# Optimization experiments

Hardware: AMD Instinct MI355X
Metric: run time of the kernel (lower is better)

Reference implementation:

```python
import jax, jax.numpy as jnp
import numpy as np

B, S, H = 1, 2048, 2048
NH, NKV, HD = 32, 4, 128
G = NH // NKV            # query groups per kv head
EPS = 1e-6
THETA = 1000000.0


def _rmsnorm(x, w):
    # per-head RMSNorm over last (head_dim) axis
    var = jnp.mean(jnp.square(x), axis=-1, keepdims=True)
    return x * jax.lax.rsqrt(var + EPS) * w


def _rotate_half(x):
    x1, x2 = jnp.split(x, 2, axis=-1)
    return jnp.concatenate([-x2, x1], axis=-1)


def _rope(x, cos, sin):
    # x: [B,S,h,HD], cos/sin: [S,HD]
    c = cos[None, :, None, :]
    s = sin[None, :, None, :]
    return x * c + _rotate_half(x) * s


def setup_inputs() -> dict:
    key = jax.random.key(0)
    ks = jax.random.split(key, 7)
    inv_freq = 1.0 / (THETA ** (jnp.arange(0, HD, 2, dtype=jnp.float32) / HD))
    freqs = jnp.outer(jnp.arange(S, dtype=jnp.float32), inv_freq)  # [S, HD/2]
    emb = jnp.concatenate([freqs, freqs], axis=-1)                 # [S, HD]
    std = 0.02
    return {
        "hidden_states": jax.random.normal(ks[0], (B, S, H), jnp.float32),
        "wq": jax.random.normal(ks[1], (H, NH * HD), jnp.float32) * std,
        "wk": jax.random.normal(ks[2], (H, NKV * HD), jnp.float32) * std,
        "wv": jax.random.normal(ks[3], (H, NKV * HD), jnp.float32) * std,
        "wo": jax.random.normal(ks[4], (NH * HD, H), jnp.float32) * std,
        "q_norm_w": jnp.ones((HD,), jnp.float32),
        "k_norm_w": jnp.ones((HD,), jnp.float32),
        "cos": jnp.cos(emb),
        "sin": jnp.sin(emb),
    }


def reference(hidden_states, wq, wk, wv, wo, q_norm_w, k_norm_w, cos, sin):
    b, s, _ = hidden_states.shape
    q = (hidden_states @ wq).reshape(b, s, NH, HD)
    k = (hidden_states @ wk).reshape(b, s, NKV, HD)
    v = (hidden_states @ wv).reshape(b, s, NKV, HD)
    # QK per-head RMSNorm, then interleaved RoPE (rotate-half form)
    q = _rope(_rmsnorm(q, q_norm_w), cos, sin)
    k = _rope(_rmsnorm(k, k_norm_w), cos, sin)
    # GQA: group Q heads per KV head instead of materializing repeated K/V
    qg = q.reshape(b, s, NKV, G, HD)
    scaling = HD ** -0.5
    scores = jnp.einsum('bqhgd,bkhd->bhgqk', qg, k) * scaling  # [B,NKV,G,S,S]
    causal = jnp.tril(jnp.ones((s, s), bool))
    scores = jnp.where(causal, scores, jnp.finfo(scores.dtype).min)
    p = jax.nn.softmax(scores, axis=-1)
    attn = jnp.einsum('bhgqk,bkhd->bqhgd', p, v).reshape(b, s, NH * HD)
    return attn @ wo
```

## Files before the change

### kernel.cpp

```cpp
#include <hip/hip_runtime.h>
#include <hip/hip_bf16.h>
#include <stdint.h>

#define SEQ 2048
#define HDIM 128
#define NHEADS 32
#define NKVH 4

typedef unsigned short u16;
typedef __bf16 bf16_t;
typedef bf16_t bf16x8 __attribute__((ext_vector_type(8)));
typedef float floatx4 __attribute__((ext_vector_type(4)));

__device__ __forceinline__ float bf2f(u16 u) {
  union { uint32_t i; float f; } v; v.i = ((uint32_t)u) << 16; return v.f;
}
__device__ __forceinline__ u16 f2bf(float f) {
  if (__builtin_isnan(f)) return 0;
  union { float f; uint32_t i; } v; v.f = f;
  uint32_t r = v.i + 0x7fffu + ((v.i >> 16) & 1u);
  return (u16)(r >> 16);
}
__device__ __forceinline__ float loadf_any(const void* p, size_t i, int isbf) {
  return isbf ? bf2f(((const u16*)p)[i]) : ((const float*)p)[i];
}

__device__ __forceinline__ void gload_lds16(const u16* g, u16* l) {
  __builtin_amdgcn_global_load_lds((__attribute__((address_space(1))) void*)g,
                                   (__attribute__((address_space(3))) void*)l,
                                   16, 0, 0);
}

__device__ __forceinline__ floatx4 mfma16(bf16x8 a, bf16x8 b, floatx4 c) {
  return __builtin_amdgcn_mfma_f32_16x16x32_bf16(a, b, c, 0, 0, 0);
}

struct InPack { const u16* p[9]; int n[9]; };

__global__ void detect_all(InPack pk, int* __restrict__ flags) {
  const int which = blockIdx.x;
  const u16* x = pk.p[which];
  const int n = pk.n[which];
  __shared__ int s_sane, s_zeven, s_zodd;
  if (threadIdx.x == 0) { s_sane = 0; s_zeven = 0; s_zodd = 0; }
  __syncthreads();
  const int ns = n < 8192 ? n : 8192;
  int sane = 0, zeven = 0, zodd = 0;
  for (int i = threadIdx.x; i < ns; i += 256) {
    const u16 u = x[i];
    const int e = (u >> 7) & 0xff;
    if ((e >= 96 && e <= 159) || u == 0) sane++;
    if (u == 0) { if (i & 1) zodd++; else zeven++; }
  }
#pragma unroll
  for (int off = 32; off >= 1; off >>= 1) {
    sane += __shfl_xor(sane, off, 64);
    zeven += __shfl_xor(zeven, off, 64);
    zodd += __shfl_xor(zodd, off, 64);
  }
  if ((threadIdx.x & 63) == 0) {
    atomicAdd(&s_sane, sane);
    atomicAdd(&s_zeven, zeven);
    atomicAdd(&s_zodd, zodd);
  }
  __syncthreads();
  if (threadIdx.x == 0) {
    const int even = (ns + 1) / 2, odd = ns / 2;
    const bool mostly_sane = (s_sane * 10 >= ns * 9);
    const bool fp32_const_pattern = (s_zeven * 2 >= even) && (s_zodd * 10 <= odd);
    flags[which] = (mostly_sane && !fp32_const_pattern) ? 1 : 0;
    if (which == 0) flags[15] = 1;
  }
}

__global__ __launch_bounds__(256) void convert_any(
    const void* __restrict__ in, u16* __restrict__ out, int n,
    const int* __restrict__ flag) {
  const int isbf = *flag;
  const int i = blockIdx.x * 256 + threadIdx.x;
  if (i >= n) return;
  out[i] = isbf ? ((const u16*)in)[i] : f2bf(((const float*)in)[i]);
}

__global__ __launch_bounds__(256) void transpose_any(
    const void* __restrict__ in, u16* __restrict__ out, int R, int C,
    const int* __restrict__ flag) {
  __shared__ u16 tile[64][65];
  const int isbf = *flag;
  const int c0 = blockIdx.x * 64, r0 = blockIdx.y * 64;
  const int t = threadIdx.x;
#pragma unroll
  for (int i = 0; i < 16; i++) {
    const int idx = i * 256 + t;
    const int r = idx >> 6, c = idx & 63;
    tile[r][c] = (u16)(isbf ? ((const u16*)in)[(size_t)(r0 + r) * C + c0 + c]
                            : f2bf(((const float*)in)[(size_t)(r0 + r) * C + c0 + c]));
  }
  __syncthreads();
#pragma unroll
  for (int i = 0; i < 16; i++) {
    const int idx = i * 256 + t;
    const int cc = idx >> 6, rr = idx & 63;
    out[(size_t)(c0 + cc) * R + r0 + rr] = tile[rr][cc];
  }
}

__global__ __launch_bounds__(256) void gemm_bt_bf16(
    const u16* __restrict__ A, const u16* __restrict__ BT,
    void* __restrict__ C, int M, int N, int K,
    const int* __restrict__ cflag) {
  __shared__ alignas(16) u16 As[128 * 32];
  __shared__ alignas(16) u16 Bs[128 * 32];
  const int t = threadIdx.x;
  const int w = t >> 6;
  const int lane = t & 63;
  const int lhi = lane >> 4, llo = lane & 15;
  const int m0 = blockIdx.y * 128, n0 = blockIdx.x * 128;
  const int wm = (w & 1) * 64, wn = (w >> 1) * 64;

  floatx4 acc[4][4];
#pragma unroll
  for (int i = 0; i < 4; i++)
#pragma unroll
    for (int j = 0; j < 4; j++) acc[i][j] = (floatx4)(0.0f);

  for (int k0 = 0; k0 < K; k0 += 32) {
#pragma unroll
    for (int r = 0; r < 2; r++) {
      const int c = r * 256 + t;
      const int row = c >> 2, kc = c & 3;
      const int base = (r * 256 + w * 64) * 8;
      gload_lds16(A + (size_t)(m0 + row) * K + k0 + kc * 8, &As[base]);
      gload_lds16(BT + (size_t)(n0 + row) * K + k0 + kc * 8, &Bs[base]);
    }
    __syncthreads();
    bf16x8 af[4], bfr[4];
#pragma unroll
    for (int i = 0; i < 4; i++)
      af[i] = *(const bf16x8*)&As[(wm + i * 16 + llo) * 32 + lhi * 8];
#pragma unroll
    for (int j = 0; j < 4; j++)
      bfr[j] = *(const bf16x8*)&Bs[(wn + j * 16 + llo) * 32 + lhi * 8];
#pragma unroll
    for (int i = 0; i < 4; i++)
#pragma unroll
      for (int j = 0; j < 4; j++)
        acc[i][j] = mfma16(af[i], bfr[j], acc[i][j]);
    __syncthreads();
  }
  const int cbf = *cflag;
#pragma unroll
  for (int i = 0; i < 4; i++) {
    const int row0 = m0 + wm + i * 16 + lhi * 4;
#pragma unroll
    for (int j = 0; j < 4; j++) {
      const int col = n0 + wn + j * 16 + llo;
#pragma unroll
      for (int r = 0; r < 4; r++) {
        if (cbf) ((u16*)C)[(size_t)(row0 + r) * N + col] = f2bf(acc[i][j][r]);
        else ((float*)C)[(size_t)(row0 + r) * N + col] = acc[i][j][r];
      }
    }
  }
}

__global__ __launch_bounds__(128) void norm_rope_inplace(
    u16* __restrict__ QKV,
    const void* __restrict__ qw, const void* __restrict__ kw,
    const void* __restrict__ cosb, const void* __restrict__ sinb,
    const int* __restrict__ flags) {
  const int qwbf = flags[5], kwbf = flags[6], cbf = flags[7], sbf = flags[8];
  const int s = blockIdx.x, hy = blockIdx.y, d = threadIdx.x;
  const bool isQ = hy < NHEADS;
  const int col = isQ ? hy * HDIM : 4096 + (hy - NHEADS) * HDIM;
  u16* ptr = QKV + (size_t)s * 5120 + col + d;
  const float x = bf2f(*ptr);
  float v = x * x;
#pragma unroll
  for (int off = 32; off >= 1; off >>= 1) v += __shfl_xor(v, off, 64);
  __shared__ float sw[2];
  __shared__ float sh[128];
  if ((d & 63) == 0) sw[d >> 6] = v;
  __syncthreads();
  const float mean = (sw[0] + sw[1]) * (1.0f / 128.0f);
  const float rn = rsqrtf(mean + 1e-6f);
  const float wv = isQ ? loadf_any(qw, d, qwbf) : loadf_any(kw, d, kwbf);
  const float xn = x * rn * wv;
  sh[d] = xn;
  __syncthreads();
  const float other = sh[d ^ 64];
  const float cv = loadf_any(cosb, (size_t)s * HDIM + d, cbf);
  const float sv = loadf_any(sinb, (size_t)s * HDIM + d, sbf);
  const float o = xn * cv + (d < 64 ? -other : other) * sv;
  *ptr = f2bf(o);
}

__global__ __launch_bounds__(256) void v_transpose(
    const u16* __restrict__ QKV, u16* __restrict__ Vt) {
  __shared__ u16 tile[64][65];
  const int s0 = blockIdx.x * 64, d0 = blockIdx.y * 64, hk = blockIdx.z;
  const int t = threadIdx.x;
#pragma unroll
  for (int i = 0; i < 16; i++) {
    const int idx = i * 256 + t;
    const int r = idx >> 6, c = idx & 63;
    tile[r][c] = QKV[(size_t)(s0 + r) * 5120 + 4608 + hk * HDIM + d0 + c];
  }
  __syncthreads();
#pragma unroll
  for (int i = 0; i < 16; i++) {
    const int idx = i * 256 + t;
    const int dd = idx >> 6, ss = idx & 63;
    Vt[((size_t)hk * HDIM + d0 + dd) * SEQ + s0 + ss] = tile[ss][dd];
  }
}

__global__ __launch_bounds__(256) void flash_attn(
    const u16* __restrict__ QKV, const u16* __restrict__ Vt,
    u16* __restrict__ O) {
  __shared__ alignas(16) u16 Klds[64 * 128];
  __shared__ alignas(16) u16 Vlds[128 * 64];
  __shared__ alignas(16) u16 Plds[4][32 * 72];
  const int t = threadIdx.x;
  const int w = t >> 6;
  const int lane = t & 63;
  const int lhi = lane >> 4, llo = lane & 15;
  const int b = blockIdx.x;
  const int qt = (SEQ / 128 - 1) - (b >> 5);
  const int h = b & 31, hk = h >> 3;
  const int q0 = qt * 128;
  const int qw0 = q0 + w * 32;
  const float scale = 0.08838834764831845f;
  const float SMAX = 16.0f;

  bf16x8 qf[2][4];
#pragma unroll
  for (int i = 0; i < 2; i++)
#pragma unroll
    for (int c = 0; c < 4; c++)
      qf[i][c] = *(const bf16x8*)(QKV + (size_t)(qw0 + i * 16 + llo) * 5120 +
                                  h * HDIM + c * 32 + lhi * 8);

  floatx4 oacc[2][8];
  float lacc[2][4];
#pragma unroll
  for (int i = 0; i < 2; i++) {
#pragma unroll
    for (int d = 0; d < 8; d++) oacc[i][d] = (floatx4)(0.0f);
#pragma unroll
    for (int r = 0; r < 4; r++) lacc[i][r] = 0.0f;
  }

  const int ntiles = 2 * qt + 2;
  for (int tt = 0; tt < ntiles; tt++) {
    const int kv0 = tt * 64;
#pragma unroll
    for (int r = 0; r < 4; r++) {
      const int c = r * 256 + t;
      const int base = (r * 256 + w * 64) * 8;
      gload_lds16(QKV + (size_t)(kv0 + (c >> 4)) * 5120 + 4096 + hk * HDIM +
                      (((c & 15) ^ ((c >> 4) & 7)) * 8),
                  &Klds[base]);
      gload_lds16(Vt + ((size_t)hk * HDIM + (c >> 3)) * SEQ + kv0 +
                      (((c & 7) ^ ((c >> 3) & 7)) * 8),
                  &Vlds[base]);
    }
    __syncthreads();

    floatx4 sacc[2][4];
#pragma unroll
    for (int i = 0; i < 2; i++)
#pragma unroll
      for (int j = 0; j < 4; j++) sacc[i][j] = (floatx4)(0.0f);
#pragma unroll
    for (int j = 0; j < 4; j++) {
#pragma unroll
      for (int c = 0; c < 4; c++) {
        bf16x8 kf = *(const bf16x8*)&Klds[(j * 16 + llo) * 128 +
                                          (((c * 4 + lhi) ^ (llo & 7)) * 8)];
        sacc[0][j] = mfma16(qf[0][c], kf, sacc[0][j]);
        sacc[1][j] = mfma16(qf[1][c], kf, sacc[1][j]);
      }
    }
    if (kv0 + 64 > q0) {
#pragma unroll
      for (int i = 0; i < 2; i++)
#pragma unroll
        for (int j = 0; j < 4; j++) {
          const int n = kv0 + j * 16 + llo;
#pragma unroll
          for (int r = 0; r < 4; r++) {
            const int mm = qw0 + i * 16 + lhi * 4 + r;
            if (n > mm) sacc[i][j][r] = -30000.0f;
          }
        }
    }
#pragma unroll
    for (int i = 0; i < 2; i++)
#pragma unroll
      for (int j = 0; j < 4; j++)
#pragma unroll
        for (int r = 0; r < 4; r++) {
          const float p = __expf(fmaf(sacc[i][j][r], scale, -SMAX));
          lacc[i][r] += p;
          Plds[w][(i * 16 + lhi * 4 + r) * 72 + j * 16 + llo] = f2bf(p);
        }
    asm volatile("" ::: "memory");
    __builtin_amdgcn_s_waitcnt(0);
    asm volatile("" ::: "memory");
#pragma unroll
    for (int c = 0; c < 2; c++) {
      bf16x8 pf0 = *(const bf16x8*)&Plds[w][llo * 72 + c * 32 + lhi * 8];
      bf16x8 pf1 = *(const bf16x8*)&Plds[w][(16 + llo) * 72 + c * 32 + lhi * 8];
#pragma unroll
      for (int d = 0; d < 8; d++) {
        bf16x8 vf = *(const bf16x8*)&Vlds[(d * 16 + llo) * 64 +
                                          (((c * 4 + lhi) ^ (llo & 7)) * 8)];
        oacc[0][d] = mfma16(pf0, vf, oacc[0][d]);
        oacc[1][d] = mfma16(pf1, vf, oacc[1][d]);
      }
    }
    __syncthreads();
  }
#pragma unroll
  for (int i = 0; i < 2; i++)
#pragma unroll
    for (int r = 0; r < 4; r++) {
#pragma unroll
      for (int off = 1; off < 16; off <<= 1)
        lacc[i][r] += __shfl_xor(lacc[i][r], off, 64);
      const float linv = 1.0f / lacc[i][r];
      const int row = qw0 + i * 16 + lhi * 4 + r;
#pragma unroll
      for (int d = 0; d < 8; d++)
        O[(size_t)row * 4096 + h * HDIM + d * 16 + llo] =
            f2bf(oacc[i][d][r] * linv);
    }
}

extern "C" void kernel_launch(void* const* d_in, const int* in_sizes, int n_in,
                              void* d_out, int out_size, void* d_ws, size_t ws_size,
                              hipStream_t stream) {
  char* ws = (char*)d_ws;
  u16* wqkvT  = (u16*)(ws);
  u16* QKVp   = (u16*)(ws + (20ull << 20));
  u16* Vt     = (u16*)(ws + (40ull << 20));
  int* flags  = (int*)(ws + (42ull << 20));
  u16* attnO  = wqkvT;
  u16* woT    = QKVp;
  u16* Hb     = (u16*)d_out;

  InPack pk;
  for (int i = 0; i < 9; i++) { pk.p[i] = (const u16*)d_in[i]; pk.n[i] = in_sizes[i]; }
  detect_all<<<9, 256, 0, stream>>>(pk, flags);

  convert_any<<<(2048 * 2048) / 256, 256, 0, stream>>>(d_in[0], Hb, 2048 * 2048, flags + 0);
  transpose_any<<<dim3(64, 32), 256, 0, stream>>>(d_in[1], wqkvT, 2048, 4096, flags + 1);
  transpose_any<<<dim3(8, 32), 256, 0, stream>>>(d_in[2], wqkvT + 4096ull * 2048, 2048, 512, flags + 2);
  transpose_any<<<dim3(8, 32), 256, 0, stream>>>(d_in[3], wqkvT + 4608ull * 2048, 2048, 512, flags + 3);

  gemm_bt_bf16<<<dim3(40, 16), 256, 0, stream>>>(
      Hb, wqkvT, QKVp, 2048, 5120, 2048, flags + 15);

  norm_rope_inplace<<<dim3(2048, NHEADS + NKVH), 128, 0, stream>>>(
      QKVp, d_in[5], d_in[6], d_in[7], d_in[8], flags);
  v_transpose<<<dim3(32, 2, 4), 256, 0, stream>>>(QKVp, Vt);

  flash_attn<<<512, 256, 0, stream>>>(QKVp, Vt, attnO);

  transpose_any<<<dim3(32, 64), 256, 0, stream>>>(d_in[4], woT, 4096, 2048, flags + 4);
  gemm_bt_bf16<<<dim3(16, 16), 256, 0, stream>>>(
      attnO, woT, d_out, 2048, 2048, 4096, flags + 0);
}
```

Measured before the change: 455.2 us.

## Fuse prep kernels, swizzle GEMM LDS, split-K output projection with atomics

Merges the dtype detection, conversion and weight-transpose launches into one multi-role prep kernel. Each block repeats the detection itself, which removes the flags buffer. XOR-swizzles the GEMM LDS layout to cut bank conflicts. Adds a split-K fp32 output GEMM that accumulates with atomics and is gated on input dtype, with a separate zeroing pass. This cuts launch count and raises parallelism for the output projection, at the cost of redundant detection work per block and atomic traffic on the output.

```diff
diff --git a/kernel.cpp b/kernel.cpp
--- a/kernel.cpp
+++ b/kernel.cpp
@@ -35,18 +35,16 @@
   return __builtin_amdgcn_mfma_f32_16x16x32_bf16(a, b, c, 0, 0, 0);
 }
 
-struct InPack { const u16* p[9]; int n[9]; };
-
-__global__ void detect_all(InPack pk, int* __restrict__ flags) {
-  const int which = blockIdx.x;
-  const u16* x = pk.p[which];
-  const int n = pk.n[which];
-  __shared__ int s_sane, s_zeven, s_zodd;
-  if (threadIdx.x == 0) { s_sane = 0; s_zeven = 0; s_zodd = 0; }
+__device__ __forceinline__ int detect_bf16_block(const u16* x, int n) {
+  __shared__ int s_cnt[3];
+  __shared__ int s_flag;
+  const int tid = threadIdx.x;
+  const int nthr = blockDim.x;
+  if (tid == 0) { s_cnt[0] = 0; s_cnt[1] = 0; s_cnt[2] = 0; }
   __syncthreads();
   const int ns = n < 8192 ? n : 8192;
   int sane = 0, zeven = 0, zodd = 0;
-  for (int i = threadIdx.x; i < ns; i += 256) {
+  for (int i = tid; i < ns; i += nthr) {
     const u16 u = x[i];
     const int e = (u >> 7) & 0xff;
     if ((e >= 96 && e <= 159) || u == 0) sane++;
@@ -58,43 +56,33 @@
     zeven += __shfl_xor(zeven, off, 64);
     zodd += __shfl_xor(zodd, off, 64);
   }
-  if ((threadIdx.x & 63) == 0) {
-    atomicAdd(&s_sane, sane);
-    atomicAdd(&s_zeven, zeven);
-    atomicAdd(&s_zodd, zodd);
+  if ((tid & 63) == 0) {
+    atomicAdd(&s_cnt[0], sane);
+    atomicAdd(&s_cnt[1], zeven);
+    atomicAdd(&s_cnt[2], zodd);
   }
   __syncthreads();
-  if (threadIdx.x == 0) {
+  if (tid == 0) {
     const int even = (ns + 1) / 2, odd = ns / 2;
-    const bool mostly_sane = (s_sane * 10 >= ns * 9);
-    const bool fp32_const_pattern = (s_zeven * 2 >= even) && (s_zodd * 10 <= odd);
-    flags[which] = (mostly_sane && !fp32_const_pattern) ? 1 : 0;
-    if (which == 0) flags[15] = 1;
-  }
-}
-
-__global__ __launch_bounds__(256) void convert_any(
-    const void* __restrict__ in, u16* __restrict__ out, int n,
-    const int* __restrict__ flag) {
-  const int isbf = *flag;
-  const int i = blockIdx.x * 256 + threadIdx.x;
-  if (i >= n) return;
-  out[i] = isbf ? ((const u16*)in)[i] : f2bf(((const float*)in)[i]);
-}
-
-__global__ __launch_bounds__(256) void transpose_any(
-    const void* __restrict__ in, u16* __restrict__ out, int R, int C,
-    const int* __restrict__ flag) {
+    const bool mostly = (s_cnt[0] * 10 >= ns * 9);
+    const bool fpconst = (s_cnt[1] * 2 >= even) && (s_cnt[2] * 10 <= odd);
+    s_flag = (mostly && !fpconst) ? 1 : 0;
+  }
+  __syncthreads();
+  return s_flag;
+}
+
+__device__ __forceinline__ void transpose_tile(
+    const void* in, u16* out, int R, int C, int bx, int by, int isbf) {
   __shared__ u16 tile[64][65];
-  const int isbf = *flag;
-  const int c0 = blockIdx.x * 64, r0 = blockIdx.y * 64;
+  const int c0 = bx * 64, r0 = by * 64;
   const int t = threadIdx.x;
 #pragma unroll
   for (int i = 0; i < 16; i++) {
     const int idx = i * 256 + t;
     const int r = idx >> 6, c = idx & 63;
-    tile[r][c] = (u16)(isbf ? ((const u16*)in)[(size_t)(r0 + r) * C + c0 + c]
-                            : f2bf(((const float*)in)[(size_t)(r0 + r) * C + c0 + c]));
+    const size_t gi = (size_t)(r0 + r) * C + c0 + c;
+    tile[r][c] = isbf ? ((const u16*)in)[gi] : f2bf(((const float*)in)[gi]);
   }
   __syncthreads();
 #pragma unroll
@@ -105,10 +93,76 @@
   }
 }
 
+struct PrepArgs {
+  const void *hidden, *wq, *wk, *wv, *cosb, *sinb, *qnw, *knw;
+  int n_hidden, n_wq, n_wk, n_wv, n_cs;
+  u16 *Hb, *wqkvT;
+  float *cosf, *sinf, *qnwf, *knwf;
+};
+
+__global__ __launch_bounds__(256) void prep1(PrepArgs a) {
+  int b = blockIdx.x;
+  if (b < 1024) {
+    const int isbf = detect_bf16_block((const u16*)a.hidden, a.n_hidden);
+    const int base = b * 4096;
+    for (int i = threadIdx.x; i < 4096; i += 256)
+      a.Hb[base + i] = isbf ? ((const u16*)a.hidden)[base + i]
+                            : f2bf(((const float*)a.hidden)[base + i]);
+    return;
+  }
+  b -= 1024;
+  if (b < 2048) {
+    const int isbf = detect_bf16_block((const u16*)a.wq, a.n_wq);
+    transpose_tile(a.wq, a.wqkvT, 2048, 4096, b & 63, b >> 6, isbf);
+    return;
+  }
+  b -= 2048;
+  if (b < 256) {
+    const int isbf = detect_bf16_block((const u16*)a.wk, a.n_wk);
+    transpose_tile(a.wk, a.wqkvT + 4096ull * 2048, 2048, 512, b & 7, b >> 3, isbf);
+    return;
+  }
+  b -= 256;
+  if (b < 256) {
+    const int isbf = detect_bf16_block((const u16*)a.wv, a.n_wv);
+    transpose_tile(a.wv, a.wqkvT + 4608ull * 2048, 2048, 512, b & 7, b >> 3, isbf);
+    return;
+  }
+  b -= 256;
+  if (b < 64) {
+    const int isbf = detect_bf16_block((const u16*)a.cosb, a.n_cs);
+    const int base = b * 4096;
+    for (int i = threadIdx.x; i < 4096; i += 256)
+      a.cosf[base + i] = loadf_any(a.cosb, base + i, isbf);
+    return;
+  }
+  b -= 64;
+  if (b < 64) {
+    const int isbf = detect_bf16_block((const u16*)a.sinb, a.n_cs);
+    const int base = b * 4096;
+    for (int i = threadIdx.x; i < 4096; i += 256)
+      a.sinf[base + i] = loadf_any(a.sinb, base + i, isbf);
+    return;
+  }
+  b -= 64;
+  if (b == 0) {
+    const int isbf = detect_bf16_block((const u16*)a.qnw, 128);
+    for (int i = threadIdx.x; i < 128; i += 256)
+      a.qnwf[i] = loadf_any(a.qnw, i, isbf);
+    return;
+  }
+  const int isbf = detect_bf16_block((const u16*)a.knw, 128);
+  for (int i = threadIdx.x; i < 128; i += 256)
+    a.knwf[i] = loadf_any(a.knw, i, isbf);
+}
+
 __global__ __launch_bounds__(256) void gemm_bt_bf16(
     const u16* __restrict__ A, const u16* __restrict__ BT,
-    void* __restrict__ C, int M, int N, int K,
-    const int* __restrict__ cflag) {
+    u16* __restrict__ C, int M, int N, int K,
+    const u16* gate, int gate_n, int gate_want) {
+  if (gate) {
+    if (detect_bf16_block(gate, gate_n) != gate_want) return;
+  }
   __shared__ alignas(16) u16 As[128 * 32];
   __shared__ alignas(16) u16 Bs[128 * 32];
   const int t = threadIdx.x;
@@ -117,6 +171,7 @@
   const int lhi = lane >> 4, llo = lane & 15;
   const int m0 = blockIdx.y * 128, n0 = blockIdx.x * 128;
   const int wm = (w & 1) * 64, wn = (w >> 1) * 64;
+  const int fg = (llo & 3) ^ ((llo >> 2) & 3);
 
   floatx4 acc[4][4];
 #pragma unroll
@@ -128,19 +183,20 @@
 #pragma unroll
     for (int r = 0; r < 2; r++) {
       const int c = r * 256 + t;
-      const int row = c >> 2, kc = c & 3;
+      const int row = c >> 2, s = c & 3;
+      const int g = (row & 3) ^ ((row >> 2) & 3);
       const int base = (r * 256 + w * 64) * 8;
-      gload_lds16(A + (size_t)(m0 + row) * K + k0 + kc * 8, &As[base]);
-      gload_lds16(BT + (size_t)(n0 + row) * K + k0 + kc * 8, &Bs[base]);
+      gload_lds16(A + (size_t)(m0 + row) * K + k0 + ((s ^ g) * 8), &As[base]);
+      gload_lds16(BT + (size_t)(n0 + row) * K + k0 + ((s ^ g) * 8), &Bs[base]);
     }
     __syncthreads();
     bf16x8 af[4], bfr[4];
 #pragma unroll
     for (int i = 0; i < 4; i++)
-      af[i] = *(const bf16x8*)&As[(wm + i * 16 + llo) * 32 + lhi * 8];
+      af[i] = *(const bf16x8*)&As[(wm + i * 16 + llo) * 32 + ((lhi ^ fg) * 8)];
 #pragma unroll
     for (int j = 0; j < 4; j++)
-      bfr[j] = *(const bf16x8*)&Bs[(wn + j * 16 + llo) * 32 + lhi * 8];
+      bfr[j] = *(const bf16x8*)&Bs[(wn + j * 16 + llo) * 32 + ((lhi ^ fg) * 8)];
 #pragma unroll
     for (int i = 0; i < 4; i++)
 #pragma unroll
@@ -148,7 +204,6 @@
         acc[i][j] = mfma16(af[i], bfr[j], acc[i][j]);
     __syncthreads();
   }
-  const int cbf = *cflag;
 #pragma unroll
   for (int i = 0; i < 4; i++) {
     const int row0 = m0 + wm + i * 16 + lhi * 4;
@@ -156,20 +211,76 @@
     for (int j = 0; j < 4; j++) {
       const int col = n0 + wn + j * 16 + llo;
 #pragma unroll
-      for (int r = 0; r < 4; r++) {
-        if (cbf) ((u16*)C)[(size_t)(row0 + r) * N + col] = f2bf(acc[i][j][r]);
-        else ((float*)C)[(size_t)(row0 + r) * N + col] = acc[i][j][r];
-      }
-    }
-  }
-}
-
-__global__ __launch_bounds__(128) void norm_rope_inplace(
-    u16* __restrict__ QKV,
-    const void* __restrict__ qw, const void* __restrict__ kw,
-    const void* __restrict__ cosb, const void* __restrict__ sinb,
-    const int* __restrict__ flags) {
-  const int qwbf = flags[5], kwbf = flags[6], cbf = flags[7], sbf = flags[8];
+      for (int r = 0; r < 4; r++)
+        C[(size_t)(row0 + r) * N + col] = f2bf(acc[i][j][r]);
+    }
+  }
+}
+
+__global__ __launch_bounds__(256) void gemm_osplit(
+    const u16* __restrict__ A, const u16* __restrict__ BT,
+    float* __restrict__ C, int M, int N, int K, int KSLICE,
+    const u16* gate, int gate_n) {
+  if (detect_bf16_block(gate, gate_n) != 0) return;
+  __shared__ alignas(16) u16 As[128 * 32];
+  __shared__ alignas(16) u16 Bs[128 * 32];
+  const int t = threadIdx.x;
+  const int w = t >> 6;
+  const int lane = t & 63;
+  const int lhi = lane >> 4, llo = lane & 15;
+  const int m0 = blockIdx.y * 128, n0 = blockIdx.x * 128;
+  const int wm = (w & 1) * 64, wn = (w >> 1) * 64;
+  const int fg = (llo & 3) ^ ((llo >> 2) & 3);
+  const int kbase = blockIdx.z * KSLICE;
+
+  floatx4 acc[4][4];
+#pragma unroll
+  for (int i = 0; i < 4; i++)
+#pragma unroll
+    for (int j = 0; j < 4; j++) acc[i][j] = (floatx4)(0.0f);
+
+  for (int k0 = kbase; k0 < kbase + KSLICE; k0 += 32) {
+#pragma unroll
+    for (int r = 0; r < 2; r++) {
+      const int c = r * 256 + t;
+      const int row = c >> 2, s = c & 3;
+      const int g = (row & 3) ^ ((row >> 2) & 3);
+      const int base = (r * 256 + w * 64) * 8;
+      gload_lds16(A + (size_t)(m0 + row) * K + k0 + ((s ^ g) * 8), &As[base]);
+      gload_lds16(BT + (size_t)(n0 + row) * K + k0 + ((s ^ g) * 8), &Bs[base]);
+    }
+    __syncthreads();
+    bf16x8 af[4], bfr[4];
+#pragma unroll
+    for (int i = 0; i < 4; i++)
+      af[i] = *(const bf16x8*)&As[(wm + i * 16 + llo) * 32 + ((lhi ^ fg) * 8)];
+#pragma unroll
+    for (int j = 0; j < 4; j++)
+      bfr[j] = *(const bf16x8*)&Bs[(wn + j * 16 + llo) * 32 + ((lhi ^ fg) * 8)];
+#pragma unroll
+    for (int i = 0; i < 4; i++)
+#pragma unroll
+      for (int j = 0; j < 4; j++)
+        acc[i][j] = mfma16(af[i], bfr[j], acc[i][j]);
+    __syncthreads();
+  }
+#pragma unroll
+  for (int i = 0; i < 4; i++) {
+    const int row0 = m0 + wm + i * 16 + lhi * 4;
+#pragma unroll
+    for (int j = 0; j < 4; j++) {
+      const int col = n0 + wn + j * 16 + llo;
+#pragma unroll
+      for (int r = 0; r < 4; r++)
+        unsafeAtomicAdd(&C[(size_t)(row0 + r) * N + col], acc[i][j][r]);
+    }
+  }
+}
+
+__global__ __launch_bounds__(128) void norm_rope(
+    u16* __restrict__ QKV, const float* __restrict__ qw,
+    const float* __restrict__ kw, const float* __restrict__ cosf,
+    const float* __restrict__ sinf) {
   const int s = blockIdx.x, hy = blockIdx.y, d = threadIdx.x;
   const bool isQ = hy < NHEADS;
   const int col = isQ ? hy * HDIM : 4096 + (hy - NHEADS) * HDIM;
@@ -184,35 +295,50 @@
   __syncthreads();
   const float mean = (sw[0] + sw[1]) * (1.0f / 128.0f);
   const float rn = rsqrtf(mean + 1e-6f);
-  const float wv = isQ ? loadf_any(qw, d, qwbf) : loadf_any(kw, d, kwbf);
+  const float wv = isQ ? qw[d] : kw[d];
   const float xn = x * rn * wv;
   sh[d] = xn;
   __syncthreads();
   const float other = sh[d ^ 64];
-  const float cv = loadf_any(cosb, (size_t)s * HDIM + d, cbf);
-  const float sv = loadf_any(sinb, (size_t)s * HDIM + d, sbf);
+  const float cv = cosf[(size_t)s * HDIM + d];
+  const float sv = sinf[(size_t)s * HDIM + d];
   const float o = xn * cv + (d < 64 ? -other : other) * sv;
   *ptr = f2bf(o);
 }
 
-__global__ __launch_bounds__(256) void v_transpose(
-    const u16* __restrict__ QKV, u16* __restrict__ Vt) {
-  __shared__ u16 tile[64][65];
-  const int s0 = blockIdx.x * 64, d0 = blockIdx.y * 64, hk = blockIdx.z;
-  const int t = threadIdx.x;
-#pragma unroll
-  for (int i = 0; i < 16; i++) {
-    const int idx = i * 256 + t;
-    const int r = idx >> 6, c = idx & 63;
-    tile[r][c] = QKV[(size_t)(s0 + r) * 5120 + 4608 + hk * HDIM + d0 + c];
-  }
-  __syncthreads();
-#pragma unroll
-  for (int i = 0; i < 16; i++) {
-    const int idx = i * 256 + t;
-    const int dd = idx >> 6, ss = idx & 63;
-    Vt[((size_t)hk * HDIM + d0 + dd) * SEQ + s0 + ss] = tile[ss][dd];
-  }
+__global__ __launch_bounds__(256) void prep2a(
+    const u16* __restrict__ QKV, u16* __restrict__ Vt,
+    float* __restrict__ outz, const u16* gate, int gate_n) {
+  int b = blockIdx.x;
+  if (b < 256) {
+    __shared__ u16 tile[64][65];
+    const int s0 = (b & 31) * 64, d0 = ((b >> 5) & 1) * 64, hk = b >> 6;
+    const int t = threadIdx.x;
+#pragma unroll
+    for (int i = 0; i < 16; i++) {
+      const int idx = i * 256 + t;
+      const int r = idx >> 6, c = idx & 63;
+      tile[r][c] = QKV[(size_t)(s0 + r) * 5120 + 4608 + hk * HDIM + d0 + c];
+    }
+    __syncthreads();
+#pragma unroll
+    for (int i = 0; i < 16; i++) {
+      const int idx = i * 256 + t;
+      const int dd = idx >> 6, ss = idx & 63;
+      Vt[((size_t)hk * HDIM + d0 + dd) * SEQ + s0 + ss] = tile[ss][dd];
+    }
+    return;
+  }
+  b -= 256;
+  if (detect_bf16_block(gate, gate_n) != 0) return;
+  const int base = b * 4096;
+  for (int i = threadIdx.x; i < 4096; i += 256) outz[base + i] = 0.0f;
+}
+
+__global__ __launch_bounds__(256) void wo_transpose(
+    const void* __restrict__ wo, u16* __restrict__ woT, int n_wo) {
+  const int isbf = detect_bf16_block((const u16*)wo, n_wo);
+  transpose_tile(wo, woT, 4096, 2048, blockIdx.x & 31, blockIdx.x >> 5, isbf);
 }
 
 __global__ __launch_bounds__(256) void flash_attn(
@@ -342,33 +468,43 @@
                               void* d_out, int out_size, void* d_ws, size_t ws_size,
                               hipStream_t stream) {
   char* ws = (char*)d_ws;
-  u16* wqkvT  = (u16*)(ws);
-  u16* QKVp   = (u16*)(ws + (20ull << 20));
-  u16* Vt     = (u16*)(ws + (40ull << 20));
-  int* flags  = (int*)(ws + (42ull << 20));
-  u16* attnO  = wqkvT;
-  u16* woT    = QKVp;
-  u16* Hb     = (u16*)d_out;
-
-  InPack pk;
-  for (int i = 0; i < 9; i++) { pk.p[i] = (const u16*)d_in[i]; pk.n[i] = in_sizes[i]; }
-  detect_all<<<9, 256, 0, stream>>>(pk, flags);
-
-  convert_any<<<(2048 * 2048) / 256, 256, 0, stream>>>(d_in[0], Hb, 2048 * 2048, flags + 0);
-  transpose_any<<<dim3(64, 32), 256, 0, stream>>>(d_in[1], wqkvT, 2048, 4096, flags + 1);
-  transpose_any<<<dim3(8, 32), 256, 0, stream>>>(d_in[2], wqkvT + 4096ull * 2048, 2048, 512, flags + 2);
-  transpose_any<<<dim3(8, 32), 256, 0, stream>>>(d_in[3], wqkvT + 4608ull * 2048, 2048, 512, flags + 3);
+  u16* wqkvT = (u16*)(ws);
+  u16* QKVp  = (u16*)(ws + (20ull << 20));
+  u16* Vt    = (u16*)(ws + (40ull << 20));
+  float* cosf = (float*)(ws + (42ull << 20));
+  float* sinf = (float*)(ws + (43ull << 20));
+  float* qnwf = (float*)(ws + (44ull << 20));
+  float* knwf = (float*)(ws + (44ull << 20) + 512);
+  u16* attnO = wqkvT;
+  u16* woT   = QKVp;
+  u16* Hb    = (u16*)d_out;
+  const u16* gate = (const u16*)d_in[0];
+  const int gate_n = in_sizes[0];
+
+  PrepArgs pa;
+  pa.hidden = d_in[0]; pa.wq = d_in[1]; pa.wk = d_in[2]; pa.wv = d_in[3];
+  pa.cosb = d_in[7]; pa.sinb = d_in[8]; pa.qnw = d_in[5]; pa.knw = d_in[6];
+  pa.n_hidden = in_sizes[0]; pa.n_wq = in_sizes[1]; pa.n_wk = in_sizes[2];
+  pa.n_wv = in_sizes[3]; pa.n_cs = in_sizes[7];
+  pa.Hb = Hb; pa.wqkvT = wqkvT;
+  pa.cosf = cosf; pa.sinf = sinf; pa.qnwf = qnwf; pa.knwf = knwf;
+
+  prep1<<<3714, 256, 0, stream>>>(pa);
 
   gemm_bt_bf16<<<dim3(40, 16), 256, 0, stream>>>(
-      Hb, wqkvT, QKVp, 2048, 5120, 2048, flags + 15);
-
-  norm_rope_inplace<<<dim3(2048, NHEADS + NKVH), 128, 0, stream>>>(
-      QKVp, d_in[5], d_in[6], d_in[7], d_in[8], flags);
-  v_transpose<<<dim3(32, 2, 4), 256, 0, stream>>>(QKVp, Vt);
+      Hb, wqkvT, QKVp, 2048, 5120, 2048, nullptr, 0, 0);
+
+  norm_rope<<<dim3(2048, NHEADS + NKVH), 128, 0, stream>>>(
+      QKVp, qnwf, knwf, cosf, sinf);
+
+  prep2a<<<1280, 256, 0, stream>>>(QKVp, Vt, (float*)d_out, gate, gate_n);
 
   flash_attn<<<512, 256, 0, stream>>>(QKVp, Vt, attnO);
 
-  transpose_any<<<dim3(32, 64), 256, 0, stream>>>(d_in[4], woT, 4096, 2048, flags + 4);
+  wo_transpose<<<2048, 256, 0, stream>>>(d_in[4], woT, in_sizes[4]);
+
+  gemm_osplit<<<dim3(16, 16, 4), 256, 0, stream>>>(
+      attnO, woT, (float*)d_out, 2048, 2048, 4096, 1024, gate, gate_n);
   gemm_bt_bf16<<<dim3(16, 16), 256, 0, stream>>>(
-      attnO, woT, d_out, 2048, 2048, 4096, flags + 0);
-}
+      attnO, woT, (u16*)d_out, 2048, 2048, 4096, gate, gate_n, 1);
+}
```

After: 503.6 us. 1.11x slower.
